# Kernel tuning notes

Hardware: AMD Instinct MI355X
Metric: run time of the kernel (lower is better)

## Reference

```python
import jax, jax.numpy as jnp
import numpy as np

B, T, IN, H = 1024, 128, 5, 100  # batch, seq_len, input_size, hidden_size


def setup_inputs() -> dict:
    key = jax.random.key(0)
    ks = jax.random.split(key, 20)
    bound = 1.0 / np.sqrt(H)  # PyTorch LSTM init: U(-1/sqrt(H), 1/sqrt(H))

    def u(k, shape):
        return jax.random.uniform(k, shape, jnp.float32, -bound, bound)

    inp = {"x": jax.random.normal(ks[0], (B, T, IN), jnp.float32)}
    i = 1
    for layer, din in [(0, IN), (1, 2 * H)]:
        for d in ("f", "b"):
            inp[f"w_ih_l{layer}{d}"] = u(ks[i], (4 * H, din)); i += 1
            inp[f"w_hh_l{layer}{d}"] = u(ks[i], (4 * H, H)); i += 1
            inp[f"b_ih_l{layer}{d}"] = u(ks[i], (4 * H,)); i += 1
            inp[f"b_hh_l{layer}{d}"] = u(ks[i], (4 * H,)); i += 1
    inp["fc_w"] = u(ks[17], (3, 2 * H))
    inp["fc_b"] = u(ks[18], (3,))
    return inp


def _run_dir(x, w_ih, w_hh, b_ih, b_hh, reverse):
    """One LSTM direction. x: [B,T,D] -> hidden seq [B,T,H]. PyTorch gate order i,f,g,o."""
    xT = jnp.swapaxes(x, 0, 1)  # [T,B,D]
    # precompute input contribution for all timesteps: [T,B,4H]
    xg = jnp.einsum('tbd,gd->tbg', xT, w_ih) + b_ih + b_hh

    def step(carry, g_in):
        h, c = carry
        g = g_in + h @ w_hh.T  # [B,4H]
        i, f, gg, o = jnp.split(g, 4, axis=-1)
        c = jax.nn.sigmoid(f) * c + jax.nn.sigmoid(i) * jnp.tanh(gg)
        h = jax.nn.sigmoid(o) * jnp.tanh(c)
        return (h, c), h

    b = x.shape[0]
    init = (jnp.zeros((b, H), x.dtype), jnp.zeros((b, H), x.dtype))
    _, hs = jax.lax.scan(step, init, xg, reverse=reverse)  # hs[t] aligned with time t
    return jnp.swapaxes(hs, 0, 1)  # [B,T,H]


def reference(x,
              w_ih_l0f, w_hh_l0f, b_ih_l0f, b_hh_l0f,
              w_ih_l0b, w_hh_l0b, b_ih_l0b, b_hh_l0b,
              w_ih_l1f, w_hh_l1f, b_ih_l1f, b_hh_l1f,
              w_ih_l1b, w_hh_l1b, b_ih_l1b, b_hh_l1b,
              fc_w, fc_b):
    # Layer 0 (bidirectional): [B,T,2H]
    h0 = jnp.concatenate([
        _run_dir(x, w_ih_l0f, w_hh_l0f, b_ih_l0f, b_hh_l0f, False),
        _run_dir(x, w_ih_l0b, w_hh_l0b, b_ih_l0b, b_hh_l0b, True),
    ], axis=-1)
    # (inter-layer dropout p=0.2 is identity in eval mode)
    # Layer 1 (bidirectional): [B,T,2H]
    h1 = jnp.concatenate([
        _run_dir(h0, w_ih_l1f, w_hh_l1f, b_ih_l1f, b_hh_l1f, False),
        _run_dir(h0, w_ih_l1b, w_hh_l1b, b_ih_l1b, b_hh_l1b, True),
    ], axis=-1)
    last = h1[:, -1, :]  # [B,2H]
    # (dropout p=0.5 is identity in eval mode)
    logits = last @ fc_w.T + fc_b  # [B,3]
    return jax.nn.softmax(logits, axis=1)
```

## Files before the change

### kernel.cpp

```cpp
#include <hip/hip_runtime.h>
#include <hip/hip_fp16.h>


typedef __attribute__((ext_vector_type(8))) short bf16x8;
typedef __attribute__((ext_vector_type(4))) float f32x4;

constexpr int Bsz = 1024, Tt = 128, IN_ = 5, H = 100, G = 400, D1 = 200;
constexpr int NP = 512;
constexpr int NT = 25;
constexpr int MB = 8;

__device__ __forceinline__ float sigm(float x)   { return 1.f / (1.f + __expf(-x)); }
__device__ __forceinline__ float tanhf_(float x) { return 1.f - 2.f / (__expf(2.f * x) + 1.f); }
__device__ __forceinline__ unsigned short f2bf(float f) {
  unsigned u = __float_as_uint(f);
  u += 0x7fff + ((u >> 16) & 1);
  return (unsigned short)(u >> 16);
}
__device__ __forceinline__ float partner8(float v) {
  return __uint_as_float(
      (unsigned)__builtin_amdgcn_ds_swizzle((int)__float_as_uint(v), 0x17));
}
__device__ __forceinline__ void barrier_nv() {
  asm volatile("s_waitcnt lgkmcnt(0)\n\ts_barrier" ::: "memory");
}

__device__ __forceinline__ void pack_body(
    const float* wA, int KA, const float* wB, int KB, int kbo,
    const float* b1, const float* b2, int bias_k,
    unsigned short* dst, int Kg, int idx) {
  if (idx >= Kg * NP * 8) return;
  int jj = idx & 7, rest = idx >> 3;
  int np_ = rest % NP, g = rest / NP;
  int j = np_ >> 2, gate = np_ & 3;
  int k = g * 8 + jj;
  float v = 0.f;
  if (j < H) {
    int n = gate * H + j;
    if (k < KA) v = wA[n * KA + k];
    else if (KB > 0 && k >= kbo && k < kbo + KB) v = wB[n * KB + (k - kbo)];
    else if (k == bias_k) v = b1[n] + b2[n];
  }
  dst[idx] = f2bf(v);
}

__global__ void pack_all(
    const float* __restrict__ w_hh_l0f, const float* __restrict__ w_ih_l0f,
    const float* __restrict__ b_ih_l0f, const float* __restrict__ b_hh_l0f,
    const float* __restrict__ w_hh_l0b, const float* __restrict__ w_ih_l0b,
    const float* __restrict__ b_ih_l0b, const float* __restrict__ b_hh_l0b,
    const float* __restrict__ w_hh_l1f, const float* __restrict__ b_ih_l1f,
    const float* __restrict__ b_hh_l1f,
    const float* __restrict__ w_ih_l1f, const float* __restrict__ w_ih_l1b,
    const float* __restrict__ b_ih_l1b, const float* __restrict__ b_hh_l1b,
    unsigned short* __restrict__ pk0f, unsigned short* __restrict__ pk0b,
    unsigned short* __restrict__ pkhh, unsigned short* __restrict__ pkxg,
    unsigned short* __restrict__ pk1b) {
  int idx = blockIdx.x * 256 + threadIdx.x;
  switch (blockIdx.y) {
    case 0: pack_body(w_hh_l0f, 100, w_ih_l0f, 5, 100, b_ih_l0f, b_hh_l0f, 105, pk0f, 16, idx); break;
    case 1: pack_body(w_hh_l0b, 100, w_ih_l0b, 5, 100, b_ih_l0b, b_hh_l0b, 105, pk0b, 16, idx); break;
    case 2: pack_body(w_hh_l1f, 100, nullptr, 0, 0, b_ih_l1f, b_hh_l1f, -1, pkhh, 16, idx); break;
    case 3: pack_body(w_ih_l1f, 200, nullptr, 0, 0, b_ih_l1f, b_hh_l1f, 200, pkxg, 28, idx); break;
    default: pack_body(w_ih_l1b, 200, nullptr, 0, 0, b_ih_l1b, b_hh_l1b, 200, pk1b, 28, idx);
  }
}

__global__ __launch_bounds__(1024, 1) void lstm_l0(
    const float* __restrict__ x,
    const unsigned short* __restrict__ pk_f, const unsigned short* __restrict__ pk_b,
    unsigned short* __restrict__ h0fT, unsigned short* __restrict__ h0bT) {
  __shared__ __align__(16) short A_s[2][16][16][8];

  const int tid = threadIdx.x;
  const int lane = tid & 63, w = tid >> 6;
  const int q = lane >> 4, l16 = lane & 15;
  const int b0 = blockIdx.x * MB;
  const int dir = blockIdx.y;
  const unsigned short* pk = dir ? pk_b : pk_f;
  unsigned short* hT = dir ? h0bT : h0fT;

  for (int i = tid; i < 2 * 16 * 16 * 8; i += 1024) ((short*)A_s)[i] = 0;

  const int mtA = w, mtB = w + 16;
  const bool bvalid = (mtB < NT);
  bf16x8 wfA[4], wfB[4];
#pragma unroll
  for (int kt = 0; kt < 4; ++kt) {
    wfA[kt] = *(const bf16x8*)(pk + ((size_t)(kt * 4 + q) * NP + mtA * 16 + l16) * 8);
    wfB[kt] = *(const bf16x8*)(pk + ((size_t)(kt * 4 + q) * NP + mtB * 16 + l16) * 8);
  }
  float c = 0.f;
  const bool up = (l16 >= 8);
  const int mm = l16 & 7;
  const int j = (up ? mtB : mtA) * 4 + q;
  const bool valid = up ? bvalid : true;
  const int xm = tid / IN_, xe = tid - xm * IN_;
  const int sm = tid / 25, sj = (tid - (tid / 25) * 25) * 4;
  const float* xp = x + ((size_t)(b0 + xm) * Tt + (dir ? Tt - 2 : 1)) * IN_ + xe;
  const int xstride = dir ? -IN_ : IN_;
  unsigned short* hp =
      hT + ((size_t)(dir ? Tt - 1 : 0) * Bsz + b0 + sm) * H + sj;
  const int hstride = dir ? -(Bsz * H) : (Bsz * H);
  __syncthreads();
  if (tid < 16) {
    A_s[0][13][tid][1] = (short)f2bf(1.f);
    A_s[1][13][tid][1] = (short)f2bf(1.f);
  }
  if (tid < MB * IN_) {
    int t0 = dir ? (Tt - 1) : 0;
    int k = 100 + xe;
    A_s[0][k >> 3][xm][k & 7] =
        (short)f2bf(x[((size_t)(b0 + xm) * Tt + t0) * IN_ + xe]);
  }
  __syncthreads();

  int p = 0;
#pragma unroll 2
  for (int step = 0; step < Tt; ++step) {
    if (step > 0 && tid < 200) {
      uint2 hv = *(const uint2*)&A_s[p][sj >> 3][sm][sj & 7];
      *(uint2*)hp = hv;
      hp += hstride;
    }
    float xn = 0.f;
    const bool do_x = (tid < MB * IN_) && (step < Tt - 1);
    if (do_x) { xn = *xp; xp += xstride; }
    bf16x8 hfrag[4];
#pragma unroll
    for (int kt = 0; kt < 4; ++kt) hfrag[kt] = *(const bf16x8*)A_s[p][kt * 4 + q][l16];
    f32x4 accA = (f32x4){0.f, 0.f, 0.f, 0.f};
    f32x4 accB = (f32x4){0.f, 0.f, 0.f, 0.f};
#pragma unroll
    for (int kt = 0; kt < 4; ++kt)
      accA = __builtin_amdgcn_mfma_f32_16x16x32_bf16(wfA[kt], hfrag[kt], accA, 0, 0, 0);
    if (bvalid) {
#pragma unroll
      for (int kt = 0; kt < 4; ++kt)
        accB = __builtin_amdgcn_mfma_f32_16x16x32_bf16(wfB[kt], hfrag[kt], accB, 0, 0, 0);
    }
    float pb0 = partner8(accB[0]), pb1 = partner8(accB[1]);
    float pb2 = partner8(accB[2]), pb3 = partner8(accB[3]);
    float g0 = up ? pb0 : accA[0];
    float g1 = up ? pb1 : accA[1];
    float g2 = up ? pb2 : accA[2];
    float g3 = up ? pb3 : accA[3];
    float cc = sigm(g1) * c + sigm(g0) * tanhf_(g2);
    c = cc;
    float h = sigm(g3) * tanhf_(cc);
    if (valid) A_s[1 - p][j >> 3][mm][j & 7] = (short)f2bf(h);
    if (do_x) {
      int k = 100 + xe;
      A_s[1 - p][k >> 3][xm][k & 7] = (short)f2bf(xn);
    }
    barrier_nv();
    p ^= 1;
  }
  if (tid < 200) *(uint2*)hp = *(const uint2*)&A_s[p][sj >> 3][sm][sj & 7];
}

__global__ __launch_bounds__(1024, 1) void gemm_xg(
    const unsigned short* __restrict__ h0fT, const unsigned short* __restrict__ h0bT,
    const unsigned short* __restrict__ pkw, __half* __restrict__ xg) {
  __shared__ __align__(16) short B_s[28][64][8];
  const int tid = threadIdx.x;
  const int lane = tid & 63, w = tid >> 6;
  const int q = lane >> 4, l16 = lane & 15;
  const int r0 = blockIdx.x * 64;
  const size_t base = (size_t)r0 * H;

  for (int i = tid; i < 3 * 64 * 8; i += 1024) {
    int jj = i & 7, gl = i >> 9;
    ((short*)&B_s[25][0][0])[i] = (short)((gl == 0 && jj == 0) ? f2bf(1.f) : 0);
  }
  for (int idx = tid; idx < 1600; idx += 1024) {
    int m = idx / 25, j0 = (idx - (idx / 25) * 25) * 4;
    *(uint2*)&B_s[j0 >> 3][m][j0 & 7] = *(const uint2*)(h0fT + base + m * H + j0);
    int k = 100 + j0;
    *(uint2*)&B_s[k >> 3][m][k & 7] = *(const uint2*)(h0bT + base + m * H + j0);
  }

  const int mtA = w, mtB = w + 16;
  const bool bvalid = (mtB < NT);
  bf16x8 wfA[7], wfB[7];
#pragma unroll
  for (int kt = 0; kt < 7; ++kt) {
    wfA[kt] = *(const bf16x8*)(pkw + ((size_t)(kt * 4 + q) * NP + mtA * 16 + l16) * 8);
    wfB[kt] = *(const bf16x8*)(pkw + ((size_t)(kt * 4 + q) * NP + mtB * 16 + l16) * 8);
  }
  const int jA = mtA * 4 + q, jB = mtB * 4 + q;
  __syncthreads();

#pragma unroll
  for (int rg = 0; rg < 4; ++rg) {
    f32x4 accA = (f32x4){0.f, 0.f, 0.f, 0.f};
    f32x4 accB = (f32x4){0.f, 0.f, 0.f, 0.f};
#pragma unroll
    for (int kt = 0; kt < 7; ++kt) {
      bf16x8 hf = *(const bf16x8*)B_s[kt * 4 + q][rg * 16 + l16];
      accA = __builtin_amdgcn_mfma_f32_16x16x32_bf16(wfA[kt], hf, accA, 0, 0, 0);
      if (bvalid)
        accB = __builtin_amdgcn_mfma_f32_16x16x32_bf16(wfB[kt], hf, accB, 0, 0, 0);
    }
    const size_t row = (size_t)(r0 + rg * 16 + l16);
    {
      __half2 h01 = __floats2half2_rn(accA[0], accA[1]);
      __half2 h23 = __floats2half2_rn(accA[2], accA[3]);
      uint2 st; *(__half2*)&st.x = h01; *(__half2*)&st.y = h23;
      *(uint2*)(xg + row * G + 4 * jA) = st;
    }
    if (bvalid) {
      __half2 h01 = __floats2half2_rn(accB[0], accB[1]);
      __half2 h23 = __floats2half2_rn(accB[2], accB[3]);
      uint2 st; *(__half2*)&st.x = h01; *(__half2*)&st.y = h23;
      *(uint2*)(xg + row * G + 4 * jB) = st;
    }
  }
}

__global__ __launch_bounds__(1024, 1) void lstm_l1(
    const unsigned short* __restrict__ h0fT, const unsigned short* __restrict__ h0bT,
    const unsigned short* __restrict__ pk_hh, const unsigned short* __restrict__ pk1b,
    const __half* __restrict__ xg,
    const float* __restrict__ fc_w, const float* __restrict__ fc_b,
    float* __restrict__ out) {
  __shared__ __align__(16) short A_s[2][16][16][8];
  __shared__ __align__(16) short A2_s[28][16][8];
  __shared__ float hf_s[MB][H];
  __shared__ float hb_s[MB][H];
  __shared__ float fcw_s[3 * D1];
  __shared__ float fcb_s[3];
  __shared__ float logit_s[MB][3];

  const int tid = threadIdx.x;
  const int lane = tid & 63, w = tid >> 6;
  const int q = lane >> 4, l16 = lane & 15;
  const int b0 = blockIdx.x * MB;
  const uint2* xg2 = (const uint2*)xg;

  for (int i = tid; i < 2 * 16 * 16 * 8; i += 1024) ((short*)A_s)[i] = 0;
  for (int i = tid; i < 25 * 16 * 8; i += 1024) ((short*)A2_s)[i] = 0;
  for (int i = tid; i < 3 * 16 * 8; i += 1024) {
    int jj = i & 7, gl = i >> 7;
    ((short*)&A2_s[25][0][0])[i] = (short)((gl == 0 && jj == 0) ? f2bf(1.f) : 0);
  }
  for (int i = tid; i < 3 * D1; i += 1024) fcw_s[i] = fc_w[i];
  if (tid < 3) fcb_s[tid] = fc_b[tid];

  const int mtA = w, mtB = w + 16;
  const bool bvalid = (mtB < NT);
  bf16x8 wfA[4], wfB[4];
#pragma unroll
  for (int kt = 0; kt < 4; ++kt) {
    wfA[kt] = *(const bf16x8*)(pk_hh + ((size_t)(kt * 4 + q) * NP + mtA * 16 + l16) * 8);
    wfB[kt] = *(const bf16x8*)(pk_hh + ((size_t)(kt * 4 + q) * NP + mtB * 16 + l16) * 8);
  }
  float c = 0.f;
  const bool up = (l16 >= 8);
  const int mm = l16 & 7;
  const int j = (up ? mtB : mtA) * 4 + q;
  const bool valid = up ? bvalid : true;
  const int jA = mtA * 4 + q;
  const int jB = mtB * 4 + q;
  const uint2* xgpA = xg2 + (size_t)(b0 + mm) * 100 + jA;
  const uint2* xgpB = xg2 + (size_t)(b0 + mm) * 100 + jB;
  uint2 xgCurA = xgpA[0], xgCurB = xgpB[0];
  xgpA += Bsz * 100; xgpB += Bsz * 100;
  float h_last = 0.f;
  __syncthreads();

  int p = 0;
#pragma unroll 2
  for (int t = 0; t < Tt; ++t) {
    uint2 xgNxtA = xgCurA, xgNxtB = xgCurB;
    if (t < Tt - 1) {
      xgNxtA = *xgpA; xgNxtB = *xgpB;
      xgpA += Bsz * 100; xgpB += Bsz * 100;
    }
    float2 a01 = __half22float2(*(const __half2*)&xgCurA.x);
    float2 a23 = __half22float2(*(const __half2*)&xgCurA.y);
    float2 b01 = __half22float2(*(const __half2*)&xgCurB.x);
    float2 b23 = __half22float2(*(const __half2*)&xgCurB.y);
    f32x4 accA = (f32x4){a01.x, a01.y, a23.x, a23.y};
    f32x4 accB = (f32x4){b01.x, b01.y, b23.x, b23.y};
    bf16x8 hfrag[4];
#pragma unroll
    for (int kt = 0; kt < 4; ++kt) hfrag[kt] = *(const bf16x8*)A_s[p][kt * 4 + q][l16];
#pragma unroll
    for (int kt = 0; kt < 4; ++kt)
      accA = __builtin_amdgcn_mfma_f32_16x16x32_bf16(wfA[kt], hfrag[kt], accA, 0, 0, 0);
    if (bvalid) {
#pragma unroll
      for (int kt = 0; kt < 4; ++kt)
        accB = __builtin_amdgcn_mfma_f32_16x16x32_bf16(wfB[kt], hfrag[kt], accB, 0, 0, 0);
    }
    float pb0 = partner8(accB[0]), pb1 = partner8(accB[1]);
    float pb2 = partner8(accB[2]), pb3 = partner8(accB[3]);
    float g0 = up ? pb0 : accA[0];
    float g1 = up ? pb1 : accA[1];
    float g2 = up ? pb2 : accA[2];
    float g3 = up ? pb3 : accA[3];
    float cc = sigm(g1) * c + sigm(g0) * tanhf_(g2);
    c = cc;
    float h = sigm(g3) * tanhf_(cc);
    if (valid) A_s[1 - p][j >> 3][mm][j & 7] = (short)f2bf(h);
    h_last = h;
    xgCurA = xgNxtA; xgCurB = xgNxtB;
    barrier_nv();
    p ^= 1;
  }
  if (valid) hf_s[mm][j] = h_last;

  {
    const size_t base = ((size_t)(Tt - 1) * Bsz + b0) * H;
    if (tid < 200) {
      int m = tid / 25, j0 = (tid - (tid / 25) * 25) * 4;
      *(uint2*)&A2_s[j0 >> 3][m][j0 & 7] = *(const uint2*)(h0fT + base + m * H + j0);
      int k = 100 + j0;
      *(uint2*)&A2_s[k >> 3][m][k & 7] = *(const uint2*)(h0bT + base + m * H + j0);
    }
  }
  __syncthreads();
  {
    f32x4 accA = (f32x4){0.f, 0.f, 0.f, 0.f};
    f32x4 accB = (f32x4){0.f, 0.f, 0.f, 0.f};
#pragma unroll
    for (int kt = 0; kt < 7; ++kt) {
      bf16x8 hf = *(const bf16x8*)A2_s[kt * 4 + q][l16];
      bf16x8 wfa = *(const bf16x8*)(pk1b + ((size_t)(kt * 4 + q) * NP + mtA * 16 + l16) * 8);
      accA = __builtin_amdgcn_mfma_f32_16x16x32_bf16(wfa, hf, accA, 0, 0, 0);
      if (bvalid) {
        bf16x8 wfb = *(const bf16x8*)(pk1b + ((size_t)(kt * 4 + q) * NP + mtB * 16 + l16) * 8);
        accB = __builtin_amdgcn_mfma_f32_16x16x32_bf16(wfb, hf, accB, 0, 0, 0);
      }
    }
    float pb0 = partner8(accB[0]);
    float pb2 = partner8(accB[2]);
    float pb3 = partner8(accB[3]);
    float g0 = up ? pb0 : accA[0];
    float g2 = up ? pb2 : accA[2];
    float g3 = up ? pb3 : accA[3];
    float cc = sigm(g0) * tanhf_(g2);
    if (valid) hb_s[mm][j] = sigm(g3) * tanhf_(cc);
  }
  __syncthreads();

  if (tid < MB * 3) {
    int m = tid / 3, cls = tid - m * 3;
    float s = fcb_s[cls];
    for (int jj = 0; jj < H; ++jj) s += fcw_s[cls * D1 + jj] * hf_s[m][jj];
    for (int jj = 0; jj < H; ++jj) s += fcw_s[cls * D1 + H + jj] * hb_s[m][jj];
    logit_s[m][cls] = s;
  }
  __syncthreads();
  if (tid < MB) {
    float a = logit_s[tid][0], b = logit_s[tid][1], cc = logit_s[tid][2];
    float mx = fmaxf(a, fmaxf(b, cc));
    float e0 = __expf(a - mx), e1 = __expf(b - mx), e2 = __expf(cc - mx);
    float inv = 1.f / (e0 + e1 + e2);
    out[(b0 + tid) * 3 + 0] = e0 * inv;
    out[(b0 + tid) * 3 + 1] = e1 * inv;
    out[(b0 + tid) * 3 + 2] = e2 * inv;
  }
}

extern "C" void kernel_launch(void* const* d_in, const int* in_sizes, int n_in,
                              void* d_out, int out_size, void* d_ws, size_t ws_size,
                              hipStream_t stream) {
  const float* x        = (const float*)d_in[0];
  const float* w_ih_l0f = (const float*)d_in[1];
  const float* w_hh_l0f = (const float*)d_in[2];
  const float* b_ih_l0f = (const float*)d_in[3];
  const float* b_hh_l0f = (const float*)d_in[4];
  const float* w_ih_l0b = (const float*)d_in[5];
  const float* w_hh_l0b = (const float*)d_in[6];
  const float* b_ih_l0b = (const float*)d_in[7];
  const float* b_hh_l0b = (const float*)d_in[8];
  const float* w_ih_l1f = (const float*)d_in[9];
  const float* w_hh_l1f = (const float*)d_in[10];
  const float* b_ih_l1f = (const float*)d_in[11];
  const float* b_hh_l1f = (const float*)d_in[12];
  const float* w_ih_l1b = (const float*)d_in[13];
  const float* b_ih_l1b = (const float*)d_in[15];
  const float* b_hh_l1b = (const float*)d_in[16];
  const float* fc_w     = (const float*)d_in[17];
  const float* fc_b     = (const float*)d_in[18];

  unsigned short* h0fT = (unsigned short*)d_ws;
  unsigned short* h0bT = h0fT + (size_t)Tt * Bsz * H;
  __half* xgT          = (__half*)(h0bT + (size_t)Tt * Bsz * H);
  unsigned short* pk0f = (unsigned short*)(xgT + (size_t)Tt * Bsz * G);
  unsigned short* pk0b = pk0f + 16 * NP * 8;
  unsigned short* pkhh = pk0b + 16 * NP * 8;
  unsigned short* pkxg = pkhh + 16 * NP * 8;
  unsigned short* pk1b = pkxg + 28 * NP * 8;

  pack_all<<<dim3(448, 5), 256, 0, stream>>>(
      w_hh_l0f, w_ih_l0f, b_ih_l0f, b_hh_l0f,
      w_hh_l0b, w_ih_l0b, b_ih_l0b, b_hh_l0b,
      w_hh_l1f, b_ih_l1f, b_hh_l1f,
      w_ih_l1f, w_ih_l1b, b_ih_l1b, b_hh_l1b,
      pk0f, pk0b, pkhh, pkxg, pk1b);

  lstm_l0<<<dim3(Bsz / MB, 2), 1024, 0, stream>>>(x, pk0f, pk0b, h0fT, h0bT);
  gemm_xg<<<(Bsz * Tt) / 64, 1024, 0, stream>>>(h0fT, h0bT, pkxg, xgT);
  lstm_l1<<<Bsz / MB, 1024, 0, stream>>>(h0fT, h0bT, pkhh, pk1b, xgT,
                                         fc_w, fc_b, (float*)d_out);
}
```

Before: 395.4 us.

## Fuse pack, layer-0, input GEMM and layer-1 into one cooperative kernel

```diff
diff --git a/kernel.cpp b/kernel.cpp
--- a/kernel.cpp
+++ b/kernel.cpp
@@ -1,5 +1,8 @@
 #include <hip/hip_runtime.h>
 #include <hip/hip_fp16.h>
+#include <hip/hip_cooperative_groups.h>
+
+namespace cg = cooperative_groups;
 
 
 typedef __attribute__((ext_vector_type(8))) short bf16x8;
@@ -28,8 +31,7 @@
 __device__ __forceinline__ void pack_body(
     const float* wA, int KA, const float* wB, int KB, int kbo,
     const float* b1, const float* b2, int bias_k,
-    unsigned short* dst, int Kg, int idx) {
-  if (idx >= Kg * NP * 8) return;
+    unsigned short* dst, int idx) {
   int jj = idx & 7, rest = idx >> 3;
   int np_ = rest % NP, g = rest / NP;
   int j = np_ >> 2, gate = np_ & 3;
@@ -44,323 +46,328 @@
   dst[idx] = f2bf(v);
 }
 
-__global__ void pack_all(
-    const float* __restrict__ w_hh_l0f, const float* __restrict__ w_ih_l0f,
+constexpr int SMEM_BYTES = 28672;
+
+__global__ __launch_bounds__(1024, 4) void lstm_mega(
+    const float* __restrict__ x,
+    const float* __restrict__ w_ih_l0f, const float* __restrict__ w_hh_l0f,
     const float* __restrict__ b_ih_l0f, const float* __restrict__ b_hh_l0f,
-    const float* __restrict__ w_hh_l0b, const float* __restrict__ w_ih_l0b,
+    const float* __restrict__ w_ih_l0b, const float* __restrict__ w_hh_l0b,
     const float* __restrict__ b_ih_l0b, const float* __restrict__ b_hh_l0b,
-    const float* __restrict__ w_hh_l1f, const float* __restrict__ b_ih_l1f,
-    const float* __restrict__ b_hh_l1f,
-    const float* __restrict__ w_ih_l1f, const float* __restrict__ w_ih_l1b,
+    const float* __restrict__ w_ih_l1f, const float* __restrict__ w_hh_l1f,
+    const float* __restrict__ b_ih_l1f, const float* __restrict__ b_hh_l1f,
+    const float* __restrict__ w_ih_l1b,
     const float* __restrict__ b_ih_l1b, const float* __restrict__ b_hh_l1b,
+    const float* __restrict__ fc_w, const float* __restrict__ fc_b,
     unsigned short* __restrict__ pk0f, unsigned short* __restrict__ pk0b,
     unsigned short* __restrict__ pkhh, unsigned short* __restrict__ pkxg,
-    unsigned short* __restrict__ pk1b) {
-  int idx = blockIdx.x * 256 + threadIdx.x;
-  switch (blockIdx.y) {
-    case 0: pack_body(w_hh_l0f, 100, w_ih_l0f, 5, 100, b_ih_l0f, b_hh_l0f, 105, pk0f, 16, idx); break;
-    case 1: pack_body(w_hh_l0b, 100, w_ih_l0b, 5, 100, b_ih_l0b, b_hh_l0b, 105, pk0b, 16, idx); break;
-    case 2: pack_body(w_hh_l1f, 100, nullptr, 0, 0, b_ih_l1f, b_hh_l1f, -1, pkhh, 16, idx); break;
-    case 3: pack_body(w_ih_l1f, 200, nullptr, 0, 0, b_ih_l1f, b_hh_l1f, 200, pkxg, 28, idx); break;
-    default: pack_body(w_ih_l1b, 200, nullptr, 0, 0, b_ih_l1b, b_hh_l1b, 200, pk1b, 28, idx);
-  }
-}
-
-__global__ __launch_bounds__(1024, 1) void lstm_l0(
-    const float* __restrict__ x,
-    const unsigned short* __restrict__ pk_f, const unsigned short* __restrict__ pk_b,
-    unsigned short* __restrict__ h0fT, unsigned short* __restrict__ h0bT) {
-  __shared__ __align__(16) short A_s[2][16][16][8];
-
+    unsigned short* __restrict__ pk1b,
+    unsigned short* __restrict__ h0fT, unsigned short* __restrict__ h0bT,
+    __half* __restrict__ xg, float* __restrict__ out) {
+  __shared__ __align__(16) char smem[SMEM_BYTES];
+  cg::grid_group grid = cg::this_grid();
+
+  const int bid = blockIdx.x;
   const int tid = threadIdx.x;
   const int lane = tid & 63, w = tid >> 6;
   const int q = lane >> 4, l16 = lane & 15;
-  const int b0 = blockIdx.x * MB;
-  const int dir = blockIdx.y;
-  const unsigned short* pk = dir ? pk_b : pk_f;
-  unsigned short* hT = dir ? h0bT : h0fT;
-
-  for (int i = tid; i < 2 * 16 * 16 * 8; i += 1024) ((short*)A_s)[i] = 0;
-
-  const int mtA = w, mtB = w + 16;
-  const bool bvalid = (mtB < NT);
-  bf16x8 wfA[4], wfB[4];
-#pragma unroll
-  for (int kt = 0; kt < 4; ++kt) {
-    wfA[kt] = *(const bf16x8*)(pk + ((size_t)(kt * 4 + q) * NP + mtA * 16 + l16) * 8);
-    wfB[kt] = *(const bf16x8*)(pk + ((size_t)(kt * 4 + q) * NP + mtB * 16 + l16) * 8);
+
+  {
+    for (int idx = bid * 1024 + tid; idx < 425984; idx += 262144) {
+      if (idx < 65536)
+        pack_body(w_hh_l0f, 100, w_ih_l0f, 5, 100, b_ih_l0f, b_hh_l0f, 105, pk0f, idx);
+      else if (idx < 131072)
+        pack_body(w_hh_l0b, 100, w_ih_l0b, 5, 100, b_ih_l0b, b_hh_l0b, 105, pk0b, idx - 65536);
+      else if (idx < 196608)
+        pack_body(w_hh_l1f, 100, nullptr, 0, 0, b_ih_l1f, b_hh_l1f, -1, pkhh, idx - 131072);
+      else if (idx < 311296)
+        pack_body(w_ih_l1f, 200, nullptr, 0, 0, b_ih_l1f, b_hh_l1f, 200, pkxg, idx - 196608);
+      else
+        pack_body(w_ih_l1b, 200, nullptr, 0, 0, b_ih_l1b, b_hh_l1b, 200, pk1b, idx - 311296);
+    }
   }
-  float c = 0.f;
-  const bool up = (l16 >= 8);
-  const int mm = l16 & 7;
-  const int j = (up ? mtB : mtA) * 4 + q;
-  const bool valid = up ? bvalid : true;
-  const int xm = tid / IN_, xe = tid - xm * IN_;
-  const int sm = tid / 25, sj = (tid - (tid / 25) * 25) * 4;
-  const float* xp = x + ((size_t)(b0 + xm) * Tt + (dir ? Tt - 2 : 1)) * IN_ + xe;
-  const int xstride = dir ? -IN_ : IN_;
-  unsigned short* hp =
-      hT + ((size_t)(dir ? Tt - 1 : 0) * Bsz + b0 + sm) * H + sj;
-  const int hstride = dir ? -(Bsz * H) : (Bsz * H);
-  __syncthreads();
-  if (tid < 16) {
-    A_s[0][13][tid][1] = (short)f2bf(1.f);
-    A_s[1][13][tid][1] = (short)f2bf(1.f);
+  __threadfence();
+  grid.sync();
+
+  {
+    auto A_s = (short(*)[16][16][8])smem;
+    const int dir = bid >> 7;
+    const int b0 = (bid & 127) * MB;
+    const unsigned short* pk = dir ? pk0b : pk0f;
+    unsigned short* hT = dir ? h0bT : h0fT;
+
+    for (int i = tid; i < 2 * 16 * 16 * 8; i += 1024) ((short*)A_s)[i] = 0;
+
+    const int mtA = w, mtB = w + 16;
+    const bool bvalid = (mtB < NT);
+    bf16x8 wfA[4], wfB[4];
+#pragma unroll
+    for (int kt = 0; kt < 4; ++kt) {
+      wfA[kt] = *(const bf16x8*)(pk + ((size_t)(kt * 4 + q) * NP + mtA * 16 + l16) * 8);
+      wfB[kt] = *(const bf16x8*)(pk + ((size_t)(kt * 4 + q) * NP + mtB * 16 + l16) * 8);
+    }
+    float c = 0.f;
+    const bool up = (l16 >= 8);
+    const int mm = l16 & 7;
+    const int j = (up ? mtB : mtA) * 4 + q;
+    const bool valid = up ? bvalid : true;
+    const int xm = tid / IN_, xe = tid - xm * IN_;
+    const int sm = tid / 25, sj = (tid - (tid / 25) * 25) * 4;
+    const float* xp = x + ((size_t)(b0 + xm) * Tt + (dir ? Tt - 2 : 1)) * IN_ + xe;
+    const int xstride = dir ? -IN_ : IN_;
+    unsigned short* hp =
+        hT + ((size_t)(dir ? Tt - 1 : 0) * Bsz + b0 + sm) * H + sj;
+    const int hstride = dir ? -(Bsz * H) : (Bsz * H);
+    __syncthreads();
+    if (tid < 16) {
+      A_s[0][13][tid][1] = (short)f2bf(1.f);
+      A_s[1][13][tid][1] = (short)f2bf(1.f);
+    }
+    if (tid < MB * IN_) {
+      int t0 = dir ? (Tt - 1) : 0;
+      int k = 100 + xe;
+      A_s[0][k >> 3][xm][k & 7] =
+          (short)f2bf(x[((size_t)(b0 + xm) * Tt + t0) * IN_ + xe]);
+    }
+    __syncthreads();
+
+    int p = 0;
+    for (int step = 0; step < Tt; ++step) {
+      if (step > 0 && tid < 200) {
+        uint2 hv = *(const uint2*)&A_s[p][sj >> 3][sm][sj & 7];
+        *(uint2*)hp = hv;
+        hp += hstride;
+      }
+      float xn = 0.f;
+      const bool do_x = (tid < MB * IN_) && (step < Tt - 1);
+      if (do_x) { xn = *xp; xp += xstride; }
+      bf16x8 hfrag[4];
+#pragma unroll
+      for (int kt = 0; kt < 4; ++kt) hfrag[kt] = *(const bf16x8*)A_s[p][kt * 4 + q][l16];
+      f32x4 accA = (f32x4){0.f, 0.f, 0.f, 0.f};
+      f32x4 accB = (f32x4){0.f, 0.f, 0.f, 0.f};
+#pragma unroll
+      for (int kt = 0; kt < 4; ++kt)
+        accA = __builtin_amdgcn_mfma_f32_16x16x32_bf16(wfA[kt], hfrag[kt], accA, 0, 0, 0);
+      if (bvalid) {
+#pragma unroll
+        for (int kt = 0; kt < 4; ++kt)
+          accB = __builtin_amdgcn_mfma_f32_16x16x32_bf16(wfB[kt], hfrag[kt], accB, 0, 0, 0);
+      }
+      float pb0 = partner8(accB[0]), pb1 = partner8(accB[1]);
+      float pb2 = partner8(accB[2]), pb3 = partner8(accB[3]);
+      float g0 = up ? pb0 : accA[0];
+      float g1 = up ? pb1 : accA[1];
+      float g2 = up ? pb2 : accA[2];
+      float g3 = up ? pb3 : accA[3];
+      float cc = sigm(g1) * c + sigm(g0) * tanhf_(g2);
+      c = cc;
+      float h = sigm(g3) * tanhf_(cc);
+      if (valid) A_s[1 - p][j >> 3][mm][j & 7] = (short)f2bf(h);
+      if (do_x) {
+        int k = 100 + xe;
+        A_s[1 - p][k >> 3][xm][k & 7] = (short)f2bf(xn);
+      }
+      barrier_nv();
+      p ^= 1;
+    }
+    if (tid < 200) *(uint2*)hp = *(const uint2*)&A_s[p][sj >> 3][sm][sj & 7];
   }
-  if (tid < MB * IN_) {
-    int t0 = dir ? (Tt - 1) : 0;
-    int k = 100 + xe;
-    A_s[0][k >> 3][xm][k & 7] =
-        (short)f2bf(x[((size_t)(b0 + xm) * Tt + t0) * IN_ + xe]);
+  __threadfence();
+  grid.sync();
+
+  {
+    auto B_s = (short(*)[64][8])smem;
+    const int mtA = w, mtB = w + 16;
+    const bool bvalid = (mtB < NT);
+    bf16x8 wfA[7], wfB[7];
+#pragma unroll
+    for (int kt = 0; kt < 7; ++kt) {
+      wfA[kt] = *(const bf16x8*)(pkxg + ((size_t)(kt * 4 + q) * NP + mtA * 16 + l16) * 8);
+      wfB[kt] = *(const bf16x8*)(pkxg + ((size_t)(kt * 4 + q) * NP + mtB * 16 + l16) * 8);
+    }
+    const int jA = mtA * 4 + q, jB = mtB * 4 + q;
+    __syncthreads();
+    for (int i = tid; i < 3 * 64 * 8; i += 1024) {
+      int jj = i & 7, gl = i >> 9;
+      ((short*)&B_s[25][0][0])[i] = (short)((gl == 0 && jj == 0) ? f2bf(1.f) : 0);
+    }
+    for (int g = 0; g < 8; ++g) {
+      const int r0 = (bid * 8 + g) * 64;
+      const size_t base = (size_t)r0 * H;
+      __syncthreads();
+      for (int idx = tid; idx < 1600; idx += 1024) {
+        int m = idx / 25, j0 = (idx - (idx / 25) * 25) * 4;
+        *(uint2*)&B_s[j0 >> 3][m][j0 & 7] = *(const uint2*)(h0fT + base + m * H + j0);
+        int k = 100 + j0;
+        *(uint2*)&B_s[k >> 3][m][k & 7] = *(const uint2*)(h0bT + base + m * H + j0);
+      }
+      __syncthreads();
+#pragma unroll
+      for (int rg = 0; rg < 4; ++rg) {
+        f32x4 accA = (f32x4){0.f, 0.f, 0.f, 0.f};
+        f32x4 accB = (f32x4){0.f, 0.f, 0.f, 0.f};
+#pragma unroll
+        for (int kt = 0; kt < 7; ++kt) {
+          bf16x8 hf = *(const bf16x8*)B_s[kt * 4 + q][rg * 16 + l16];
+          accA = __builtin_amdgcn_mfma_f32_16x16x32_bf16(wfA[kt], hf, accA, 0, 0, 0);
+          if (bvalid)
+            accB = __builtin_amdgcn_mfma_f32_16x16x32_bf16(wfB[kt], hf, accB, 0, 0, 0);
+        }
+        const size_t row = (size_t)(r0 + rg * 16 + l16);
+        {
+          __half2 h01 = __floats2half2_rn(accA[0], accA[1]);
+          __half2 h23 = __floats2half2_rn(accA[2], accA[3]);
+          uint2 st; *(__half2*)&st.x = h01; *(__half2*)&st.y = h23;
+          *(uint2*)(xg + row * G + 4 * jA) = st;
+        }
+        if (bvalid) {
+          __half2 h01 = __floats2half2_rn(accB[0], accB[1]);
+          __half2 h23 = __floats2half2_rn(accB[2], accB[3]);
+          uint2 st; *(__half2*)&st.x = h01; *(__half2*)&st.y = h23;
+          *(uint2*)(xg + row * G + 4 * jB) = st;
+        }
+      }
+    }
   }
-  __syncthreads();
-
-  int p = 0;
-#pragma unroll 2
-  for (int step = 0; step < Tt; ++step) {
-    if (step > 0 && tid < 200) {
-      uint2 hv = *(const uint2*)&A_s[p][sj >> 3][sm][sj & 7];
-      *(uint2*)hp = hv;
-      hp += hstride;
-    }
-    float xn = 0.f;
-    const bool do_x = (tid < MB * IN_) && (step < Tt - 1);
-    if (do_x) { xn = *xp; xp += xstride; }
-    bf16x8 hfrag[4];
-#pragma unroll
-    for (int kt = 0; kt < 4; ++kt) hfrag[kt] = *(const bf16x8*)A_s[p][kt * 4 + q][l16];
-    f32x4 accA = (f32x4){0.f, 0.f, 0.f, 0.f};
-    f32x4 accB = (f32x4){0.f, 0.f, 0.f, 0.f};
-#pragma unroll
-    for (int kt = 0; kt < 4; ++kt)
-      accA = __builtin_amdgcn_mfma_f32_16x16x32_bf16(wfA[kt], hfrag[kt], accA, 0, 0, 0);
-    if (bvalid) {
+  __threadfence();
+  grid.sync();
+
+  if (bid < 128) {
+    auto A_s  = (short(*)[16][16][8])smem;
+    auto A2_s = (short(*)[16][8])(smem + 8192);
+    float* hf_s   = (float*)(smem + 15360);
+    float* hb_s   = (float*)(smem + 18560);
+    float* fcw_s  = (float*)(smem + 21760);
+    float* fcb_s  = (float*)(smem + 24160);
+    float* logit_s = (float*)(smem + 24176);
+
+    const int b0 = bid * MB;
+    const uint2* xg2 = (const uint2*)xg;
+
+    for (int i = tid; i < 2 * 16 * 16 * 8; i += 1024) ((short*)A_s)[i] = 0;
+    for (int i = tid; i < 25 * 16 * 8; i += 1024) ((short*)A2_s)[i] = 0;
+    for (int i = tid; i < 3 * 16 * 8; i += 1024) {
+      int jj = i & 7, gl = i >> 7;
+      ((short*)&A2_s[25][0][0])[i] = (short)((gl == 0 && jj == 0) ? f2bf(1.f) : 0);
+    }
+    for (int i = tid; i < 3 * D1; i += 1024) fcw_s[i] = fc_w[i];
+    if (tid < 3) fcb_s[tid] = fc_b[tid];
+
+    const int mtA = w, mtB = w + 16;
+    const bool bvalid = (mtB < NT);
+    bf16x8 wfA[4], wfB[4];
+#pragma unroll
+    for (int kt = 0; kt < 4; ++kt) {
+      wfA[kt] = *(const bf16x8*)(pkhh + ((size_t)(kt * 4 + q) * NP + mtA * 16 + l16) * 8);
+      wfB[kt] = *(const bf16x8*)(pkhh + ((size_t)(kt * 4 + q) * NP + mtB * 16 + l16) * 8);
+    }
+    float c = 0.f;
+    const bool up = (l16 >= 8);
+    const int mm = l16 & 7;
+    const int j = (up ? mtB : mtA) * 4 + q;
+    const bool valid = up ? bvalid : true;
+    const int jA = mtA * 4 + q;
+    const int jB = mtB * 4 + q;
+    const uint2* xgpA = xg2 + (size_t)(b0 + mm) * 100 + jA;
+    const uint2* xgpB = xg2 + (size_t)(b0 + mm) * 100 + jB;
+    uint2 xgCurA = xgpA[0], xgCurB = xgpB[0];
+    xgpA += Bsz * 100; xgpB += Bsz * 100;
+    float h_last = 0.f;
+    __syncthreads();
+
+    int p = 0;
+    for (int t = 0; t < Tt; ++t) {
+      uint2 xgNxtA = xgCurA, xgNxtB = xgCurB;
+      if (t < Tt - 1) {
+        xgNxtA = *xgpA; xgNxtB = *xgpB;
+        xgpA += Bsz * 100; xgpB += Bsz * 100;
+      }
+      float2 a01 = __half22float2(*(const __half2*)&xgCurA.x);
+      float2 a23 = __half22float2(*(const __half2*)&xgCurA.y);
+      float2 b01 = __half22float2(*(const __half2*)&xgCurB.x);
+      float2 b23 = __half22float2(*(const __half2*)&xgCurB.y);
+      f32x4 accA = (f32x4){a01.x, a01.y, a23.x, a23.y};
+      f32x4 accB = (f32x4){b01.x, b01.y, b23.x, b23.y};
+      bf16x8 hfrag[4];
+#pragma unroll
+      for (int kt = 0; kt < 4; ++kt) hfrag[kt] = *(const bf16x8*)A_s[p][kt * 4 + q][l16];
 #pragma unroll
       for (int kt = 0; kt < 4; ++kt)
-        accB = __builtin_amdgcn_mfma_f32_16x16x32_bf16(wfB[kt], hfrag[kt], accB, 0, 0, 0);
-    }
-    float pb0 = partner8(accB[0]), pb1 = partner8(accB[1]);
-    float pb2 = partner8(accB[2]), pb3 = partner8(accB[3]);
-    float g0 = up ? pb0 : accA[0];
-    float g1 = up ? pb1 : accA[1];
-    float g2 = up ? pb2 : accA[2];
-    float g3 = up ? pb3 : accA[3];
-    float cc = sigm(g1) * c + sigm(g0) * tanhf_(g2);
-    c = cc;
-    float h = sigm(g3) * tanhf_(cc);
-    if (valid) A_s[1 - p][j >> 3][mm][j & 7] = (short)f2bf(h);
-    if (do_x) {
-      int k = 100 + xe;
-      A_s[1 - p][k >> 3][xm][k & 7] = (short)f2bf(xn);
-    }
-    barrier_nv();
-    p ^= 1;
-  }
-  if (tid < 200) *(uint2*)hp = *(const uint2*)&A_s[p][sj >> 3][sm][sj & 7];
-}
-
-__global__ __launch_bounds__(1024, 1) void gemm_xg(
-    const unsigned short* __restrict__ h0fT, const unsigned short* __restrict__ h0bT,
-    const unsigned short* __restrict__ pkw, __half* __restrict__ xg) {
-  __shared__ __align__(16) short B_s[28][64][8];
-  const int tid = threadIdx.x;
-  const int lane = tid & 63, w = tid >> 6;
-  const int q = lane >> 4, l16 = lane & 15;
-  const int r0 = blockIdx.x * 64;
-  const size_t base = (size_t)r0 * H;
-
-  for (int i = tid; i < 3 * 64 * 8; i += 1024) {
-    int jj = i & 7, gl = i >> 9;
-    ((short*)&B_s[25][0][0])[i] = (short)((gl == 0 && jj == 0) ? f2bf(1.f) : 0);
-  }
-  for (int idx = tid; idx < 1600; idx += 1024) {
-    int m = idx / 25, j0 = (idx - (idx / 25) * 25) * 4;
-    *(uint2*)&B_s[j0 >> 3][m][j0 & 7] = *(const uint2*)(h0fT + base + m * H + j0);
-    int k = 100 + j0;
-    *(uint2*)&B_s[k >> 3][m][k & 7] = *(const uint2*)(h0bT + base + m * H + j0);
-  }
-
-  const int mtA = w, mtB = w + 16;
-  const bool bvalid = (mtB < NT);
-  bf16x8 wfA[7], wfB[7];
-#pragma unroll
-  for (int kt = 0; kt < 7; ++kt) {
-    wfA[kt] = *(const bf16x8*)(pkw + ((size_t)(kt * 4 + q) * NP + mtA * 16 + l16) * 8);
-    wfB[kt] = *(const bf16x8*)(pkw + ((size_t)(kt * 4 + q) * NP + mtB * 16 + l16) * 8);
-  }
-  const int jA = mtA * 4 + q, jB = mtB * 4 + q;
-  __syncthreads();
-
-#pragma unroll
-  for (int rg = 0; rg < 4; ++rg) {
-    f32x4 accA = (f32x4){0.f, 0.f, 0.f, 0.f};
-    f32x4 accB = (f32x4){0.f, 0.f, 0.f, 0.f};
-#pragma unroll
-    for (int kt = 0; kt < 7; ++kt) {
-      bf16x8 hf = *(const bf16x8*)B_s[kt * 4 + q][rg * 16 + l16];
-      accA = __builtin_amdgcn_mfma_f32_16x16x32_bf16(wfA[kt], hf, accA, 0, 0, 0);
-      if (bvalid)
-        accB = __builtin_amdgcn_mfma_f32_16x16x32_bf16(wfB[kt], hf, accB, 0, 0, 0);
-    }
-    const size_t row = (size_t)(r0 + rg * 16 + l16);
+        accA = __builtin_amdgcn_mfma_f32_16x16x32_bf16(wfA[kt], hfrag[kt], accA, 0, 0, 0);
+      if (bvalid) {
+#pragma unroll
+        for (int kt = 0; kt < 4; ++kt)
+          accB = __builtin_amdgcn_mfma_f32_16x16x32_bf16(wfB[kt], hfrag[kt], accB, 0, 0, 0);
+      }
+      float pb0 = partner8(accB[0]), pb1 = partner8(accB[1]);
+      float pb2 = partner8(accB[2]), pb3 = partner8(accB[3]);
+      float g0 = up ? pb0 : accA[0];
+      float g1 = up ? pb1 : accA[1];
+      float g2 = up ? pb2 : accA[2];
+      float g3 = up ? pb3 : accA[3];
+      float cc = sigm(g1) * c + sigm(g0) * tanhf_(g2);
+      c = cc;
+      float h = sigm(g3) * tanhf_(cc);
+      if (valid) A_s[1 - p][j >> 3][mm][j & 7] = (short)f2bf(h);
+      h_last = h;
+      xgCurA = xgNxtA; xgCurB = xgNxtB;
+      barrier_nv();
+      p ^= 1;
+    }
+    if (valid) hf_s[mm * H + j] = h_last;
+
     {
-      __half2 h01 = __floats2half2_rn(accA[0], accA[1]);
-      __half2 h23 = __floats2half2_rn(accA[2], accA[3]);
-      uint2 st; *(__half2*)&st.x = h01; *(__half2*)&st.y = h23;
-      *(uint2*)(xg + row * G + 4 * jA) = st;
-    }
-    if (bvalid) {
-      __half2 h01 = __floats2half2_rn(accB[0], accB[1]);
-      __half2 h23 = __floats2half2_rn(accB[2], accB[3]);
-      uint2 st; *(__half2*)&st.x = h01; *(__half2*)&st.y = h23;
-      *(uint2*)(xg + row * G + 4 * jB) = st;
-    }
-  }
-}
-
-__global__ __launch_bounds__(1024, 1) void lstm_l1(
-    const unsigned short* __restrict__ h0fT, const unsigned short* __restrict__ h0bT,
-    const unsigned short* __restrict__ pk_hh, const unsigned short* __restrict__ pk1b,
-    const __half* __restrict__ xg,
-    const float* __restrict__ fc_w, const float* __restrict__ fc_b,
-    float* __restrict__ out) {
-  __shared__ __align__(16) short A_s[2][16][16][8];
-  __shared__ __align__(16) short A2_s[28][16][8];
-  __shared__ float hf_s[MB][H];
-  __shared__ float hb_s[MB][H];
-  __shared__ float fcw_s[3 * D1];
-  __shared__ float fcb_s[3];
-  __shared__ float logit_s[MB][3];
-
-  const int tid = threadIdx.x;
-  const int lane = tid & 63, w = tid >> 6;
-  const int q = lane >> 4, l16 = lane & 15;
-  const int b0 = blockIdx.x * MB;
-  const uint2* xg2 = (const uint2*)xg;
-
-  for (int i = tid; i < 2 * 16 * 16 * 8; i += 1024) ((short*)A_s)[i] = 0;
-  for (int i = tid; i < 25 * 16 * 8; i += 1024) ((short*)A2_s)[i] = 0;
-  for (int i = tid; i < 3 * 16 * 8; i += 1024) {
-    int jj = i & 7, gl = i >> 7;
-    ((short*)&A2_s[25][0][0])[i] = (short)((gl == 0 && jj == 0) ? f2bf(1.f) : 0);
-  }
-  for (int i = tid; i < 3 * D1; i += 1024) fcw_s[i] = fc_w[i];
-  if (tid < 3) fcb_s[tid] = fc_b[tid];
-
-  const int mtA = w, mtB = w + 16;
-  const bool bvalid = (mtB < NT);
-  bf16x8 wfA[4], wfB[4];
-#pragma unroll
-  for (int kt = 0; kt < 4; ++kt) {
-    wfA[kt] = *(const bf16x8*)(pk_hh + ((size_t)(kt * 4 + q) * NP + mtA * 16 + l16) * 8);
-    wfB[kt] = *(const bf16x8*)(pk_hh + ((size_t)(kt * 4 + q) * NP + mtB * 16 + l16) * 8);
-  }
-  float c = 0.f;
-  const bool up = (l16 >= 8);
-  const int mm = l16 & 7;
-  const int j = (up ? mtB : mtA) * 4 + q;
-  const bool valid = up ? bvalid : true;
-  const int jA = mtA * 4 + q;
-  const int jB = mtB * 4 + q;
-  const uint2* xgpA = xg2 + (size_t)(b0 + mm) * 100 + jA;
-  const uint2* xgpB = xg2 + (size_t)(b0 + mm) * 100 + jB;
-  uint2 xgCurA = xgpA[0], xgCurB = xgpB[0];
-  xgpA += Bsz * 100; xgpB += Bsz * 100;
-  float h_last = 0.f;
-  __syncthreads();
-
-  int p = 0;
-#pragma unroll 2
-  for (int t = 0; t < Tt; ++t) {
-    uint2 xgNxtA = xgCurA, xgNxtB = xgCurB;
-    if (t < Tt - 1) {
-      xgNxtA = *xgpA; xgNxtB = *xgpB;
-      xgpA += Bsz * 100; xgpB += Bsz * 100;
-    }
-    float2 a01 = __half22float2(*(const __half2*)&xgCurA.x);
-    float2 a23 = __half22float2(*(const __half2*)&xgCurA.y);
-    float2 b01 = __half22float2(*(const __half2*)&xgCurB.x);
-    float2 b23 = __half22float2(*(const __half2*)&xgCurB.y);
-    f32x4 accA = (f32x4){a01.x, a01.y, a23.x, a23.y};
-    f32x4 accB = (f32x4){b01.x, b01.y, b23.x, b23.y};
-    bf16x8 hfrag[4];
-#pragma unroll
-    for (int kt = 0; kt < 4; ++kt) hfrag[kt] = *(const bf16x8*)A_s[p][kt * 4 + q][l16];
-#pragma unroll
-    for (int kt = 0; kt < 4; ++kt)
-      accA = __builtin_amdgcn_mfma_f32_16x16x32_bf16(wfA[kt], hfrag[kt], accA, 0, 0, 0);
-    if (bvalid) {
-#pragma unroll
-      for (int kt = 0; kt < 4; ++kt)
-        accB = __builtin_amdgcn_mfma_f32_16x16x32_bf16(wfB[kt], hfrag[kt], accB, 0, 0, 0);
-    }
-    float pb0 = partner8(accB[0]), pb1 = partner8(accB[1]);
-    float pb2 = partner8(accB[2]), pb3 = partner8(accB[3]);
-    float g0 = up ? pb0 : accA[0];
-    float g1 = up ? pb1 : accA[1];
-    float g2 = up ? pb2 : accA[2];
-    float g3 = up ? pb3 : accA[3];
-    float cc = sigm(g1) * c + sigm(g0) * tanhf_(g2);
-    c = cc;
-    float h = sigm(g3) * tanhf_(cc);
-    if (valid) A_s[1 - p][j >> 3][mm][j & 7] = (short)f2bf(h);
-    h_last = h;
-    xgCurA = xgNxtA; xgCurB = xgNxtB;
-    barrier_nv();
-    p ^= 1;
-  }
-  if (valid) hf_s[mm][j] = h_last;
-
-  {
-    const size_t base = ((size_t)(Tt - 1) * Bsz + b0) * H;
-    if (tid < 200) {
-      int m = tid / 25, j0 = (tid - (tid / 25) * 25) * 4;
-      *(uint2*)&A2_s[j0 >> 3][m][j0 & 7] = *(const uint2*)(h0fT + base + m * H + j0);
-      int k = 100 + j0;
-      *(uint2*)&A2_s[k >> 3][m][k & 7] = *(const uint2*)(h0bT + base + m * H + j0);
-    }
-  }
-  __syncthreads();
-  {
-    f32x4 accA = (f32x4){0.f, 0.f, 0.f, 0.f};
-    f32x4 accB = (f32x4){0.f, 0.f, 0.f, 0.f};
-#pragma unroll
-    for (int kt = 0; kt < 7; ++kt) {
-      bf16x8 hf = *(const bf16x8*)A2_s[kt * 4 + q][l16];
-      bf16x8 wfa = *(const bf16x8*)(pk1b + ((size_t)(kt * 4 + q) * NP + mtA * 16 + l16) * 8);
-      accA = __builtin_amdgcn_mfma_f32_16x16x32_bf16(wfa, hf, accA, 0, 0, 0);
-      if (bvalid) {
-        bf16x8 wfb = *(const bf16x8*)(pk1b + ((size_t)(kt * 4 + q) * NP + mtB * 16 + l16) * 8);
-        accB = __builtin_amdgcn_mfma_f32_16x16x32_bf16(wfb, hf, accB, 0, 0, 0);
-      }
-    }
-    float pb0 = partner8(accB[0]);
-    float pb2 = partner8(accB[2]);
-    float pb3 = partner8(accB[3]);
-    float g0 = up ? pb0 : accA[0];
-    float g2 = up ? pb2 : accA[2];
-    float g3 = up ? pb3 : accA[3];
-    float cc = sigm(g0) * tanhf_(g2);
-    if (valid) hb_s[mm][j] = sigm(g3) * tanhf_(cc);
-  }
-  __syncthreads();
-
-  if (tid < MB * 3) {
-    int m = tid / 3, cls = tid - m * 3;
-    float s = fcb_s[cls];
-    for (int jj = 0; jj < H; ++jj) s += fcw_s[cls * D1 + jj] * hf_s[m][jj];
-    for (int jj = 0; jj < H; ++jj) s += fcw_s[cls * D1 + H + jj] * hb_s[m][jj];
-    logit_s[m][cls] = s;
-  }
-  __syncthreads();
-  if (tid < MB) {
-    float a = logit_s[tid][0], b = logit_s[tid][1], cc = logit_s[tid][2];
-    float mx = fmaxf(a, fmaxf(b, cc));
-    float e0 = __expf(a - mx), e1 = __expf(b - mx), e2 = __expf(cc - mx);
-    float inv = 1.f / (e0 + e1 + e2);
-    out[(b0 + tid) * 3 + 0] = e0 * inv;
-    out[(b0 + tid) * 3 + 1] = e1 * inv;
-    out[(b0 + tid) * 3 + 2] = e2 * inv;
+      const size_t base = ((size_t)(Tt - 1) * Bsz + b0) * H;
+      if (tid < 200) {
+        int m = tid / 25, j0 = (tid - (tid / 25) * 25) * 4;
+        *(uint2*)&A2_s[j0 >> 3][m][j0 & 7] = *(const uint2*)(h0fT + base + m * H + j0);
+        int k = 100 + j0;
+        *(uint2*)&A2_s[k >> 3][m][k & 7] = *(const uint2*)(h0bT + base + m * H + j0);
+      }
+    }
+    __syncthreads();
+    {
+      f32x4 accA = (f32x4){0.f, 0.f, 0.f, 0.f};
+      f32x4 accB = (f32x4){0.f, 0.f, 0.f, 0.f};
+#pragma unroll
+      for (int kt = 0; kt < 7; ++kt) {
+        bf16x8 hf = *(const bf16x8*)A2_s[kt * 4 + q][l16];
+        bf16x8 wfa = *(const bf16x8*)(pk1b + ((size_t)(kt * 4 + q) * NP + mtA * 16 + l16) * 8);
+        accA = __builtin_amdgcn_mfma_f32_16x16x32_bf16(wfa, hf, accA, 0, 0, 0);
+        if (bvalid) {
+          bf16x8 wfb = *(const bf16x8*)(pk1b + ((size_t)(kt * 4 + q) * NP + mtB * 16 + l16) * 8);
+          accB = __builtin_amdgcn_mfma_f32_16x16x32_bf16(wfb, hf, accB, 0, 0, 0);
+        }
+      }
+      float pb0 = partner8(accB[0]);
+      float pb2 = partner8(accB[2]);
+      float pb3 = partner8(accB[3]);
+      float g0 = up ? pb0 : accA[0];
+      float g2 = up ? pb2 : accA[2];
+      float g3 = up ? pb3 : accA[3];
+      float cc = sigm(g0) * tanhf_(g2);
+      if (valid) hb_s[mm * H + j] = sigm(g3) * tanhf_(cc);
+    }
+    __syncthreads();
+
+    if (tid < MB * 3) {
+      int m = tid / 3, cls = tid - m * 3;
+      float s = fcb_s[cls];
+      for (int jj = 0; jj < H; ++jj) s += fcw_s[cls * D1 + jj] * hf_s[m * H + jj];
+      for (int jj = 0; jj < H; ++jj) s += fcw_s[cls * D1 + H + jj] * hb_s[m * H + jj];
+      logit_s[m * 3 + cls] = s;
+    }
+    __syncthreads();
+    if (tid < MB) {
+      float a = logit_s[tid * 3 + 0], b = logit_s[tid * 3 + 1], cc = logit_s[tid * 3 + 2];
+      float mx = fmaxf(a, fmaxf(b, cc));
+      float e0 = __expf(a - mx), e1 = __expf(b - mx), e2 = __expf(cc - mx);
+      float inv = 1.f / (e0 + e1 + e2);
+      out[(b0 + tid) * 3 + 0] = e0 * inv;
+      out[(b0 + tid) * 3 + 1] = e1 * inv;
+      out[(b0 + tid) * 3 + 2] = e2 * inv;
+    }
   }
 }
 
@@ -394,16 +401,18 @@
   unsigned short* pkhh = pk0b + 16 * NP * 8;
   unsigned short* pkxg = pkhh + 16 * NP * 8;
   unsigned short* pk1b = pkxg + 28 * NP * 8;
-
-  pack_all<<<dim3(448, 5), 256, 0, stream>>>(
-      w_hh_l0f, w_ih_l0f, b_ih_l0f, b_hh_l0f,
-      w_hh_l0b, w_ih_l0b, b_ih_l0b, b_hh_l0b,
-      w_hh_l1f, b_ih_l1f, b_hh_l1f,
-      w_ih_l1f, w_ih_l1b, b_ih_l1b, b_hh_l1b,
-      pk0f, pk0b, pkhh, pkxg, pk1b);
-
-  lstm_l0<<<dim3(Bsz / MB, 2), 1024, 0, stream>>>(x, pk0f, pk0b, h0fT, h0bT);
-  gemm_xg<<<(Bsz * Tt) / 64, 1024, 0, stream>>>(h0fT, h0bT, pkxg, xgT);
-  lstm_l1<<<Bsz / MB, 1024, 0, stream>>>(h0fT, h0bT, pkhh, pk1b, xgT,
-                                         fc_w, fc_b, (float*)d_out);
-}
+  float* outp = (float*)d_out;
+
+  void* kargs[] = {
+    (void*)&x,
+    (void*)&w_ih_l0f, (void*)&w_hh_l0f, (void*)&b_ih_l0f, (void*)&b_hh_l0f,
+    (void*)&w_ih_l0b, (void*)&w_hh_l0b, (void*)&b_ih_l0b, (void*)&b_hh_l0b,
+    (void*)&w_ih_l1f, (void*)&w_hh_l1f, (void*)&b_ih_l1f, (void*)&b_hh_l1f,
+    (void*)&w_ih_l1b, (void*)&b_ih_l1b, (void*)&b_hh_l1b,
+    (void*)&fc_w, (void*)&fc_b,
+    (void*)&pk0f, (void*)&pk0b, (void*)&pkhh, (void*)&pkxg, (void*)&pk1b,
+    (void*)&h0fT, (void*)&h0bT, (void*)&xgT, (void*)&outp,
+  };
+  hipLaunchCooperativeKernel((void*)lstm_mega, dim3(256), dim3(1024),
+                             kargs, 0, stream);
+}
```

Measured after the change: 724.4 us. 1.83x slower.
